# Kernel tuning notes

Hardware: AMD Instinct MI355X
Metric: run time of the kernel (lower is better)

## Reference

```python
import jax, jax.numpy as jnp
import numpy as np

NUM_HEAD = 8


def setup_inputs() -> dict:
    key = jax.random.key(0)
    ks = jax.random.split(key, 9)
    B, C, H, W = 4, 32, 1024, 64  # [batch, dim_input, Input_len, nodes]
    s = 1.0 / np.sqrt(C)
    return {
        "x": jax.random.normal(ks[0], (B, C, H, W), dtype=jnp.float32),
        # 1x1 conv weights stored as [out, in]
        "wq": jax.random.normal(ks[1], (C, C), dtype=jnp.float32) * s,
        "bq": jax.random.normal(ks[2], (C,), dtype=jnp.float32) * 0.01,
        "wk": jax.random.normal(ks[3], (C, C), dtype=jnp.float32) * s,
        "bk": jax.random.normal(ks[4], (C,), dtype=jnp.float32) * 0.01,
        "wv": jax.random.normal(ks[5], (C, C), dtype=jnp.float32) * s,
        "bv": jax.random.normal(ks[6], (C,), dtype=jnp.float32) * 0.01,
        # nn.Linear(num_head, 1): weight [1, num_head], bias [1]
        "w_lin": jax.random.normal(ks[7], (1, NUM_HEAD), dtype=jnp.float32) * (1.0 / np.sqrt(NUM_HEAD)),
        "b_lin": jax.random.normal(ks[8], (1,), dtype=jnp.float32) * 0.01,
    }


def reference(x, wq, bq, wk, bk, wv, bv, w_lin, b_lin):
    # x: [B, C, H, W]; 1x1 conv == channel matmul
    def conv1x1(w, b):
        return jnp.einsum("bchw,oc->bohw", x, w) + b[None, :, None, None]

    # transpose(-3,-1): [B, C, H, W] -> [B, W, H, C]
    q = conv1x1(wq, bq).transpose(0, 3, 2, 1)  # [B, W, H, C]
    k = conv1x1(wk, bk).transpose(0, 3, 2, 1)  # [B, W, H, C]
    v = conv1x1(wv, bv).transpose(0, 3, 2, 1)  # [B, W, H, C]

    H = x.shape[2]
    kd = jnp.sqrt(jnp.float32(H) / NUM_HEAD)
    scores = jnp.einsum("bwhc,bwgc->bwhg", q, k) / kd  # [B, W, H, H]
    attn = jax.nn.softmax(scores, axis=-1)
    line = jnp.einsum("bwhg,bwgc->bwhc", attn, v)  # [B, W, H, C]

    # All num_head heads share weights (dropout=identity at eval), so
    # linear1 over the stacked-head axis == line * sum(w_lin) + b_lin.
    result = line * jnp.sum(w_lin) + b_lin[0]
    # squeeze(-1) then transpose(1,3): [B, W, H, C] -> [B, C, H, W]
    return result.transpose(0, 3, 2, 1)
```

## Files before the change

kernel.cpp:

```cpp
#include <hip/hip_runtime.h>

typedef unsigned short u16;
typedef unsigned int   u32;
typedef __bf16 bf16x8 __attribute__((ext_vector_type(8)));
typedef float  f32x4  __attribute__((ext_vector_type(4)));

#define KSCALE 0.12751743f

__device__ __forceinline__ u32 cvtpk(float lo, float hi) {
    u32 r;
    asm("v_cvt_pk_bf16_f32 %0, %1, %2" : "=v"(r) : "v"(lo), "v"(hi));
    return r;
}

__global__ __launch_bounds__(256, 4) void qkv_proj(
    const float* __restrict__ x,
    const float* __restrict__ wq, const float* __restrict__ bq,
    const float* __restrict__ wk, const float* __restrict__ bk,
    const float* __restrict__ wv, const float* __restrict__ bv,
    u16* __restrict__ Qb, u16* __restrict__ Kb, u16* __restrict__ Vb)
{
    __shared__ __align__(16) u16 sW[3][32][40];
    __shared__ float sB[3][32];
    __shared__ __align__(16) u16 sO[8192];
    const int tid = threadIdx.x;
    const int b  = blockIdx.x >> 8;
    const int h0 = (blockIdx.x & 255) * 4;
    const int wid = tid >> 6, lane = tid & 63;
    const int g = lane >> 4, c = lane & 15;

    {
        const float* Ws[3] = {wq, wk, wv};
#pragma unroll
        for (int m = 0; m < 3; m++) {
            const float sc = (m == 1) ? KSCALE : 1.0f;
            for (int i = tid; i < 512; i += 256) {
                float2 v = ((const float2*)Ws[m])[i];
                int co = i >> 4, cip = i & 15;
                ((u32*)&sW[m][co][0])[cip] = cvtpk(v.x * sc, v.y * sc);
            }
        }
        if (tid < 96) {
            const float* Bs[3] = {bq, bk, bv};
            float v = Bs[tid >> 5][tid & 31];
            if ((tid >> 5) == 1) v *= KSCALE;
            ((float*)sB)[tid] = v;
        }
    }

    bf16x8 xf[4];
    {
        const float* xb = x + (size_t)b * 2097152 + (size_t)h0 * 64 + wid * 64;
#pragma unroll
        for (int pt = 0; pt < 4; pt++) {
            float f[8];
#pragma unroll
            for (int j = 0; j < 8; j++)
                f[j] = xb[(size_t)(8 * g + j) * 65536 + pt * 16 + c];
            uint4 u;
            u.x = cvtpk(f[0], f[1]); u.y = cvtpk(f[2], f[3]);
            u.z = cvtpk(f[4], f[5]); u.w = cvtpk(f[6], f[7]);
            xf[pt] = __builtin_bit_cast(bf16x8, u);
        }
    }
    __syncthreads();

    u16* outs[3] = {Qb, Kb, Vb};
    const f32x4 zz = {0.f, 0.f, 0.f, 0.f};

#pragma unroll
    for (int m = 0; m < 3; m++) {
        bf16x8 wf[2];
        float4 bias[2];
#pragma unroll
        for (int a = 0; a < 2; a++) {
            wf[a] = __builtin_bit_cast(bf16x8,
                *(const uint4*)((const char*)&sW[m][a * 16 + c][0] + g * 16));
            bias[a] = *(const float4*)&sB[m][a * 16 + g * 4];
        }

        f32x4 o[2][4];
#pragma unroll
        for (int a = 0; a < 2; a++)
#pragma unroll
            for (int pt = 0; pt < 4; pt++)
                o[a][pt] = __builtin_amdgcn_mfma_f32_16x16x32_bf16(wf[a], xf[pt], zz, 0, 0, 0);

        if (m) __syncthreads();

#pragma unroll
        for (int a = 0; a < 2; a++)
#pragma unroll
            for (int pt = 0; pt < 4; pt++) {
                int w = pt * 16 + c;
                float v0 = o[a][pt][0] + bias[a].x;
                float v1 = o[a][pt][1] + bias[a].y;
                float v2 = o[a][pt][2] + bias[a].z;
                float v3 = o[a][pt][3] + bias[a].w;
                uint2 st;
                st.x = cvtpk(v0, v1);
                st.y = cvtpk(v2, v3);
                int chunk = (wid * 4 + a * 2 + (g >> 1)) ^ (w & 7);
                *(uint2*)((char*)sO + w * 256 + chunk * 16 + (g & 1) * 8) = st;
            }
        __syncthreads();

        u16* gout = outs[m];
#pragma unroll
        for (int i = 0; i < 4; i++) {
            int L = tid + i * 256;
            int w_ = L >> 4, lc = L & 15;
            uint4 val = *(const uint4*)((const char*)sO + w_ * 256 + ((lc ^ (w_ & 7)) << 4));
            int hh = lc >> 2, sub = lc & 3;
            size_t off;
            if (m == 1) {
                int kv = h0 + hh;
                int q5 = kv & 31;
                int slot = (kv & ~31) | ((q5 & 4) << 2) | ((q5 & 24) >> 1) | (q5 & 3);
                off = (size_t)(b * 64 + w_) * 32768 + slot * 32 + (sub ^ ((slot >> 1) & 3)) * 8;
            } else {
                off = (size_t)(b * 64 + w_) * 32768 + (h0 + hh) * 32 + sub * 8;
            }
            *(uint4*)(gout + off) = val;
        }
    }
}

__global__ __launch_bounds__(1024, 4) void attn(
    const u16* __restrict__ Qb, const u16* __restrict__ Kb,
    const u16* __restrict__ Vb, float* __restrict__ Ow)
{
    __shared__ __align__(16) char sK[65536];
    __shared__ __align__(16) char sV[65536];
    const int tid = threadIdx.x;
    const int p = blockIdx.x;

    {
        const uint4* gK = (const uint4*)(Kb + (size_t)p * 32768);
        uint4* sK4 = (uint4*)sK;
        for (int m = tid; m < 4096; m += 1024)
            sK4[m] = gK[m];
        const uint4* gV = (const uint4*)(Vb + (size_t)p * 32768);
        for (int m = tid; m < 4096; m += 1024) {
            uint4 val = gV[m];
            int kv = m >> 2, c0 = (m & 3) * 8;
            const u16* pv = (const u16*)&val;
#pragma unroll
            for (int k = 0; k < 8; k++) {
                int d = c0 + k;
                int chv = (kv >> 3) ^ (d & 7) ^ ((d >> 3) & 3);
                *(u16*)(sV + d * 2048 + (chv << 4) + (kv & 7) * 2) = pv[k];
            }
        }
    }
    __syncthreads();

    const int wid = tid >> 6, lane = tid & 63;
    const int g = lane >> 4, c = lane & 15;

    bf16x8 qf[4];
    {
        const u16* qbase = Qb + (size_t)p * 32768;
#pragma unroll
        for (int nq = 0; nq < 4; nq++) {
            int row = wid * 64 + nq * 16 + c;
            qf[nq] = __builtin_bit_cast(bf16x8, *(const uint4*)(qbase + row * 32 + g * 8));
        }
    }

    f32x4 o[4][2];
    float lsum[4];
    const f32x4 zz = {0.f, 0.f, 0.f, 0.f};
#pragma unroll
    for (int nq = 0; nq < 4; nq++) { o[nq][0] = zz; o[nq][1] = zz; lsum[nq] = 0.f; }

    for (int j = 0; j < 32; j++) {
        const int kv0 = j * 32;
        const int ra = kv0 + c;
        const int rb = ra + 16;
        bf16x8 k0 = __builtin_bit_cast(bf16x8,
            *(const uint4*)(sK + ra * 64 + ((g ^ ((ra >> 1) & 3)) << 4)));
        bf16x8 k1 = __builtin_bit_cast(bf16x8,
            *(const uint4*)(sK + rb * 64 + ((g ^ ((rb >> 1) & 3)) << 4)));
        const int cb = (kv0 >> 3) + g;
        bf16x8 v0 = __builtin_bit_cast(bf16x8,
            *(const uint4*)(sV + c * 2048 + ((cb ^ (c & 7) ^ ((c >> 3) & 3)) << 4)));
        bf16x8 v1 = __builtin_bit_cast(bf16x8,
            *(const uint4*)(sV + (c + 16) * 2048 + ((cb ^ (c & 7) ^ (((c + 16) >> 3) & 3)) << 4)));

#pragma unroll
        for (int nq = 0; nq < 4; nq++) {
            f32x4 s0 = __builtin_amdgcn_mfma_f32_16x16x32_bf16(k0, qf[nq], zz, 0, 0, 0);
            f32x4 s1 = __builtin_amdgcn_mfma_f32_16x16x32_bf16(k1, qf[nq], zz, 0, 0, 0);
            float p0[4], p1[4];
#pragma unroll
            for (int r = 0; r < 4; r++) {
                p0[r] = __builtin_amdgcn_exp2f(s0[r]);
                p1[r] = __builtin_amdgcn_exp2f(s1[r]);
            }
            lsum[nq] += (p0[0] + p0[1] + p0[2] + p0[3]) + (p1[0] + p1[1] + p1[2] + p1[3]);
            uint4 pw;
            pw.x = cvtpk(p0[0], p0[1]);
            pw.y = cvtpk(p0[2], p0[3]);
            pw.z = cvtpk(p1[0], p1[1]);
            pw.w = cvtpk(p1[2], p1[3]);
            bf16x8 pf = __builtin_bit_cast(bf16x8, pw);
            o[nq][0] = __builtin_amdgcn_mfma_f32_16x16x32_bf16(v0, pf, o[nq][0], 0, 0, 0);
            o[nq][1] = __builtin_amdgcn_mfma_f32_16x16x32_bf16(v1, pf, o[nq][1], 0, 0, 0);
        }
    }

#pragma unroll
    for (int nq = 0; nq < 4; nq++) {
        float s = lsum[nq];
        s += __shfl_xor(s, 16, 64);
        s += __shfl_xor(s, 32, 64);
        const float inv = 1.0f / s;
        const int hq = wid * 64 + nq * 16 + c;
        float* dst = Ow + (size_t)p * 32768 + hq;
#pragma unroll
        for (int t = 0; t < 2; t++)
#pragma unroll
            for (int r = 0; r < 4; r++) {
                int d = t * 16 + g * 4 + r;
                dst[(size_t)d * 1024] = o[nq][t][r] * inv;
            }
    }
}

__global__ __launch_bounds__(256) void finalize_tr(
    const float* __restrict__ Ow, const float* __restrict__ w_lin,
    const float* __restrict__ b_lin, float* __restrict__ out)
{
    __shared__ float tile[64][65];
    const int tid = threadIdx.x;
    const int bi = blockIdx.x;
    const int b = bi >> 9, d = (bi >> 4) & 31, ht = bi & 15;
    const int h0 = ht * 64;

    float slin = 0.f;
#pragma unroll
    for (int i = 0; i < 8; i++) slin += w_lin[i];
    const float bl = b_lin[0];

    const int w = tid >> 2, part = tid & 3;
    const float4* src = (const float4*)(Ow + (((size_t)b * 64 + w) * 32 + d) * 1024 + h0 + part * 16);
#pragma unroll
    for (int i = 0; i < 4; i++) {
        float4 v = src[i];
        int hh = part * 16 + i * 4;
        tile[w][hh + 0] = v.x; tile[w][hh + 1] = v.y;
        tile[w][hh + 2] = v.z; tile[w][hh + 3] = v.w;
    }
    __syncthreads();

    const int ww = tid & 63, hb = tid >> 6;
    const size_t obase = ((size_t)b * 32 + d) * 1024 + h0;
#pragma unroll
    for (int k = 0; k < 16; k++) {
        int hh = k * 4 + hb;
        out[(obase + hh) * 64 + ww] = tile[ww][hh] * slin + bl;
    }
}

extern "C" void kernel_launch(void* const* d_in, const int* in_sizes, int n_in,
                              void* d_out, int out_size, void* d_ws, size_t ws_size,
                              hipStream_t stream)
{
    const float* x  = (const float*)d_in[0];
    const float* wq = (const float*)d_in[1];
    const float* bq = (const float*)d_in[2];
    const float* wk = (const float*)d_in[3];
    const float* bk = (const float*)d_in[4];
    const float* wv = (const float*)d_in[5];
    const float* bv = (const float*)d_in[6];
    const float* wl = (const float*)d_in[7];
    const float* bl = (const float*)d_in[8];
    float* out = (float*)d_out;

    char* ws = (char*)d_ws;
    u16*   Qb = (u16*)(ws);
    u16*   Kb = (u16*)(ws + (16u << 20));
    u16*   Vb = (u16*)(ws + (32u << 20));
    float* Ow = (float*)(ws + (48u << 20));

    qkv_proj<<<1024, 256, 0, stream>>>(x, wq, bq, wk, bk, wv, bv, Qb, Kb, Vb);
    attn<<<256, 1024, 0, stream>>>(Qb, Kb, Vb, Ow);
    finalize_tr<<<2048, 256, 0, stream>>>(Ow, wl, bl, out);
}
```

Baseline: 75.61 us.

## Compute softmax row sums via MFMA with ones and batch phases with sched barriers

Replaces the per-lane scalar accumulation of exp values (plus cross-lane shuffles) with an extra MFMA against a ones vector, so the row sum comes out of the matrix unit using the same bf16-rounded probabilities as the PV product. The inner loop is split into three phases (all QK MFMAs, all exp/convert, all PV MFMAs) separated by sched_barrier, so the VALU and matrix work is grouped to give more independent instructions. It also relaxes the launch bound from 4 to 2 blocks per CU to give the compiler more register room. The cost is a third more PV-stage MFMAs, more live registers for the batched score fragments, and possibly lower occupancy.

```diff
diff --git a/kernel.cpp b/kernel.cpp
--- a/kernel.cpp
+++ b/kernel.cpp
@@ -126,7 +126,7 @@
     }
 }
 
-__global__ __launch_bounds__(1024, 4) void attn(
+__global__ __launch_bounds__(1024, 2) void attn(
     const u16* __restrict__ Qb, const u16* __restrict__ Kb,
     const u16* __restrict__ Vb, float* __restrict__ Ow)
 {
@@ -168,11 +168,17 @@
         }
     }
 
+    bf16x8 ones;
+    {
+        uint4 u; u.x = u.y = u.z = u.w = 0x3F803F80u;
+        ones = __builtin_bit_cast(bf16x8, u);
+    }
+
     f32x4 o[4][2];
-    float lsum[4];
+    f32x4 ls[4];
     const f32x4 zz = {0.f, 0.f, 0.f, 0.f};
 #pragma unroll
-    for (int nq = 0; nq < 4; nq++) { o[nq][0] = zz; o[nq][1] = zz; lsum[nq] = 0.f; }
+    for (int nq = 0; nq < 4; nq++) { o[nq][0] = zz; o[nq][1] = zz; ls[nq] = zz; }
 
     for (int j = 0; j < 32; j++) {
         const int kv0 = j * 32;
@@ -188,34 +194,43 @@
         bf16x8 v1 = __builtin_bit_cast(bf16x8,
             *(const uint4*)(sV + (c + 16) * 2048 + ((cb ^ (c & 7) ^ (((c + 16) >> 3) & 3)) << 4)));
 
+        f32x4 sA[4], sB_[4];
 #pragma unroll
         for (int nq = 0; nq < 4; nq++) {
-            f32x4 s0 = __builtin_amdgcn_mfma_f32_16x16x32_bf16(k0, qf[nq], zz, 0, 0, 0);
-            f32x4 s1 = __builtin_amdgcn_mfma_f32_16x16x32_bf16(k1, qf[nq], zz, 0, 0, 0);
+            sA[nq]  = __builtin_amdgcn_mfma_f32_16x16x32_bf16(k0, qf[nq], zz, 0, 0, 0);
+            sB_[nq] = __builtin_amdgcn_mfma_f32_16x16x32_bf16(k1, qf[nq], zz, 0, 0, 0);
+        }
+        __builtin_amdgcn_sched_barrier(0);
+
+        bf16x8 pf[4];
+#pragma unroll
+        for (int nq = 0; nq < 4; nq++) {
             float p0[4], p1[4];
 #pragma unroll
             for (int r = 0; r < 4; r++) {
-                p0[r] = __builtin_amdgcn_exp2f(s0[r]);
-                p1[r] = __builtin_amdgcn_exp2f(s1[r]);
-            }
-            lsum[nq] += (p0[0] + p0[1] + p0[2] + p0[3]) + (p1[0] + p1[1] + p1[2] + p1[3]);
+                p0[r] = __builtin_amdgcn_exp2f(sA[nq][r]);
+                p1[r] = __builtin_amdgcn_exp2f(sB_[nq][r]);
+            }
             uint4 pw;
             pw.x = cvtpk(p0[0], p0[1]);
             pw.y = cvtpk(p0[2], p0[3]);
             pw.z = cvtpk(p1[0], p1[1]);
             pw.w = cvtpk(p1[2], p1[3]);
-            bf16x8 pf = __builtin_bit_cast(bf16x8, pw);
-            o[nq][0] = __builtin_amdgcn_mfma_f32_16x16x32_bf16(v0, pf, o[nq][0], 0, 0, 0);
-            o[nq][1] = __builtin_amdgcn_mfma_f32_16x16x32_bf16(v1, pf, o[nq][1], 0, 0, 0);
+            pf[nq] = __builtin_bit_cast(bf16x8, pw);
+        }
+        __builtin_amdgcn_sched_barrier(0);
+
+#pragma unroll
+        for (int nq = 0; nq < 4; nq++) {
+            o[nq][0] = __builtin_amdgcn_mfma_f32_16x16x32_bf16(v0, pf[nq], o[nq][0], 0, 0, 0);
+            o[nq][1] = __builtin_amdgcn_mfma_f32_16x16x32_bf16(v1, pf[nq], o[nq][1], 0, 0, 0);
+            ls[nq]   = __builtin_amdgcn_mfma_f32_16x16x32_bf16(ones, pf[nq], ls[nq], 0, 0, 0);
         }
     }
 
 #pragma unroll
     for (int nq = 0; nq < 4; nq++) {
-        float s = lsum[nq];
-        s += __shfl_xor(s, 16, 64);
-        s += __shfl_xor(s, 32, 64);
-        const float inv = 1.0f / s;
+        const float inv = 1.0f / ls[nq][0];
         const int hq = wid * 64 + nq * 16 + c;
         float* dst = Ow + (size_t)p * 32768 + hq;
 #pragma unroll
```

Measured after the change: 73.65 us. 1.03x faster.
